# Optimization experiments

Measured on AMD Instinct MI355X. Metric: run time of the kernel, lower is better.

The kernel has to match this reference:

```python
import jax, jax.numpy as jnp
import numpy as np

N_NODES = 100000
N_EDGES = 3200000
N_GRAPHS = 64
IN_DIM = 64
LATENT = 64
DIST_STD = 1.0


def _gcn_conv(x, W, b, src, dst, dinv):
    """PyG GCNConv: out = D^-1/2 (A+I) D^-1/2 (x W) + b, with dinv = deg^-1/2."""
    n = x.shape[0]
    h = x @ W  # [N, out]
    coef = dinv[src] * dinv[dst]  # per-edge norm
    agg = jax.ops.segment_sum(h[src] * coef[:, None], dst, num_segments=n)
    # self-loop contribution with norm dinv[i]^2
    return agg + h * (dinv * dinv)[:, None] + b


def _mean_pool(x, batch, num_graphs):
    sums = jax.ops.segment_sum(x, batch, num_segments=num_graphs)
    cnts = jax.ops.segment_sum(jnp.ones((x.shape[0],), x.dtype), batch, num_segments=num_graphs)
    return sums / jnp.maximum(cnts, 1.0)[:, None]


def setup_inputs() -> dict:
    key = jax.random.key(0)
    ks = jax.random.split(key, 12)
    x = jax.random.normal(ks[0], (N_NODES, IN_DIM), jnp.float32)
    edge_index = jax.random.randint(ks[1], (2, N_EDGES), 0, N_NODES, jnp.int64 if jax.config.jax_enable_x64 else jnp.int32).astype(jnp.int32)
    batch = jnp.sort(jax.random.randint(ks[2], (N_NODES,), 0, N_GRAPHS)).astype(jnp.int32)

    def glorot(k, shape):
        fan_in, fan_out = shape
        s = jnp.sqrt(6.0 / (fan_in + fan_out))
        return jax.random.uniform(k, shape, jnp.float32, -s, s)

    return {
        "x": x, "edge_index": edge_index, "batch": batch,
        "W1m": glorot(ks[3], (IN_DIM, 16)), "b1m": jnp.zeros((16,), jnp.float32),
        "W2m": glorot(ks[4], (16, 32)), "b2m": jnp.zeros((32,), jnp.float32),
        "W3m": glorot(ks[5], (32, LATENT)), "b3m": jnp.zeros((LATENT,), jnp.float32),
        "W1l": glorot(ks[6], (IN_DIM, 16)), "b1l": jnp.zeros((16,), jnp.float32),
        "W2l": glorot(ks[7], (16, 32)), "b2l": jnp.zeros((32,), jnp.float32),
        "W3l": glorot(ks[8], (32, LATENT)), "b3l": jnp.zeros((LATENT,), jnp.float32),
        "Wfc": glorot(ks[9], (LATENT, 160000)), "bfc": jnp.zeros((160000,), jnp.float32),
        "eps": jax.random.normal(ks[10], (N_GRAPHS, LATENT), jnp.float32) * DIST_STD,
    }


def reference(x, edge_index, batch, W1m, b1m, W2m, b2m, W3m, b3m,
              W1l, b1l, W2l, b2l, W3l, b3l, Wfc, bfc, eps):
    src, dst = edge_index[0], edge_index[1]
    n = x.shape[0]
    # degrees include self-loop (+1)
    deg = jax.ops.segment_sum(jnp.ones((src.shape[0],), x.dtype), dst, num_segments=n) + 1.0
    dinv = jax.lax.rsqrt(deg)

    mu = jax.nn.relu(_gcn_conv(x, W1m, b1m, src, dst, dinv))
    mu = jax.nn.relu(_gcn_conv(mu, W2m, b2m, src, dst, dinv))
    mu = jax.nn.relu(_gcn_conv(mu, W3m, b3m, src, dst, dinv))
    mu = _mean_pool(mu, batch, N_GRAPHS)

    log = jax.nn.relu(_gcn_conv(x, W1l, b1l, src, dst, dinv))
    log = jax.nn.relu(_gcn_conv(log, W2l, b2l, src, dst, dinv))
    log = jax.nn.relu(_gcn_conv(log, W3l, b3l, src, dst, dinv))
    logvar = _mean_pool(log, batch, N_GRAPHS)

    # latent sample (training mode): z = mu + eps * exp(0.5*logvar)
    z = mu + eps * jnp.exp(0.5 * logvar)

    # decode: sigmoid(z Wfc + bfc) -> [G, 400, 400]
    output = jax.nn.sigmoid(z @ Wfc + bfc).reshape(-1, 400, 400)
    return output, mu, logvar
```

## Files before the change

### kernel.cpp

```cpp
#include <hip/hip_runtime.h>
#include <hip/hip_bf16.h>

#define N_NODES 100000
#define N_EDGES 3200000
#define N_GRAPHS 64
#define NB 391
#define KCH 8192
#define NCHUNK ((N_EDGES + KCH - 1) / KCH)
#define MAXBKT 10240

__device__ __forceinline__ void atomAddF(float* p, float v) {
    unsafeAtomicAdd(p, v);
}

__device__ __forceinline__ float lo2f(unsigned u) { return __uint_as_float(u << 16); }
__device__ __forceinline__ float hi2f(unsigned u) { return __uint_as_float(u & 0xFFFF0000u); }
__device__ __forceinline__ unsigned pack2(float a, float b) {
    unsigned ha = __bfloat16_as_ushort(__float2bfloat16(a));
    unsigned hb = __bfloat16_as_ushort(__float2bfloat16(b));
    return ha | (hb << 16);
}

__global__ __launch_bounds__(512) void k_binCount(const int* __restrict__ dst,
                                                  int* __restrict__ gcount) {
    __shared__ int hist[NB];
    for (int t = threadIdx.x; t < NB; t += 512) hist[t] = 0;
    __syncthreads();
    int base = blockIdx.x * KCH;
    int cnt = min(KCH, N_EDGES - base);
    for (int i = threadIdx.x; i < cnt; i += 512)
        atomicAdd(&hist[dst[base + i] >> 8], 1);
    __syncthreads();
    for (int t = threadIdx.x; t < NB; t += 512)
        if (hist[t]) atomicAdd(&gcount[t], hist[t]);
}

__global__ __launch_bounds__(512) void k_scanB(const int* __restrict__ gcount,
                                               int* __restrict__ gbase,
                                               int* __restrict__ gcursor,
                                               int* __restrict__ rowptr) {
    __shared__ int s[512];
    int v = (threadIdx.x < NB) ? gcount[threadIdx.x] : 0;
    s[threadIdx.x] = v;
    __syncthreads();
    for (int off = 1; off < 512; off <<= 1) {
        int t = (threadIdx.x >= off) ? s[threadIdx.x - off] : 0;
        __syncthreads();
        s[threadIdx.x] += t;
        __syncthreads();
    }
    if (threadIdx.x < NB) {
        int e = s[threadIdx.x] - v;
        gbase[threadIdx.x] = e;
        gcursor[threadIdx.x] = e;
    }
    if (threadIdx.x == 0) rowptr[N_NODES] = N_EDGES;
}

__global__ __launch_bounds__(512) void k_binA(const int* __restrict__ src,
                                              const int* __restrict__ dst,
                                              int* __restrict__ gcursor,
                                              int* __restrict__ binned) {
    __shared__ int hist[512];
    __shared__ int sc[512];
    __shared__ int sexc[512];
    __shared__ int rbase[512];
    __shared__ int stage[KCH];
    hist[threadIdx.x] = 0;
    __syncthreads();
    int base = blockIdx.x * KCH;
    int cnt = min(KCH, N_EDGES - base);
    int myb[16], mypos[16];
    int nmine = 0;
    for (int i = 0; i < 16; ++i) {
        int idx = i * 512 + threadIdx.x;
        if (idx < cnt) {
            int b = dst[base + idx] >> 8;
            myb[nmine] = b;
            mypos[nmine] = atomicAdd(&hist[b], 1);
            ++nmine;
        }
    }
    __syncthreads();
    int v = hist[threadIdx.x];
    sc[threadIdx.x] = v;
    __syncthreads();
    for (int off = 1; off < 512; off <<= 1) {
        int t = (threadIdx.x >= off) ? sc[threadIdx.x - off] : 0;
        __syncthreads();
        sc[threadIdx.x] += t;
        __syncthreads();
    }
    sexc[threadIdx.x] = sc[threadIdx.x] - v;
    __syncthreads();
    if (threadIdx.x < NB && v > 0)
        rbase[threadIdx.x] = atomicAdd(&gcursor[threadIdx.x], v);
    for (int k = 0; k < nmine; ++k) {
        int e = base + k * 512 + threadIdx.x;
        int p = ((dst[e] & 255) << 24) | src[e];
        stage[sexc[myb[k]] + mypos[k]] = p;
    }
    __syncthreads();
    for (int j = threadIdx.x; j < cnt; j += 512) {
        int lo = 0, hi = NB - 1;
        while (lo < hi) {
            int mid = (lo + hi + 1) >> 1;
            if (sexc[mid] <= j) lo = mid; else hi = mid - 1;
        }
        binned[rbase[lo] + (j - sexc[lo])] = stage[j];
    }
}

__global__ __launch_bounds__(512) void k_passB(const int* __restrict__ gbase,
                                               int* __restrict__ csr,
                                               int* __restrict__ rowptr,
                                               float* __restrict__ dinv) {
    int b = blockIdx.x;
    int rb = gbase[b];
    int re = (b == NB - 1) ? N_EDGES : gbase[b + 1];
    int cnt = re - rb;
    int nbase = b << 8;
    int nn = min(nbase + 256, N_NODES) - nbase;
    __shared__ int stage[MAXBKT];
    __shared__ int nhist[256];
    __shared__ int sc[256];
    __shared__ int ncur[256];
    for (int t = threadIdx.x; t < 256; t += 512) nhist[t] = 0;
    __syncthreads();
    for (int j = threadIdx.x; j < cnt; j += 512) {
        int p = csr[rb + j];
        stage[j] = p;
        atomicAdd(&nhist[((unsigned)p) >> 24], 1);
    }
    __syncthreads();
    if (threadIdx.x < 256) sc[threadIdx.x] = nhist[threadIdx.x];
    __syncthreads();
    for (int off = 1; off < 256; off <<= 1) {
        int t = (threadIdx.x < 256 && threadIdx.x >= off) ? sc[threadIdx.x - off] : 0;
        __syncthreads();
        if (threadIdx.x < 256) sc[threadIdx.x] += t;
        __syncthreads();
    }
    if (threadIdx.x < 256) {
        int e = sc[threadIdx.x] - nhist[threadIdx.x];
        ncur[threadIdx.x] = e;
        if (threadIdx.x < nn) {
            rowptr[nbase + threadIdx.x] = rb + e;
            dinv[nbase + threadIdx.x] = rsqrtf((float)nhist[threadIdx.x] + 1.0f);
        }
    }
    __syncthreads();
    for (int j = threadIdx.x; j < cnt; j += 512) {
        int p = stage[j];
        int slot = atomicAdd(&ncur[((unsigned)p) >> 24], 1);
        csr[rb + slot] = p;
    }
}

template<int LOGW, bool BIAS_RELU, bool OB, bool PRE>
__global__ void __launch_bounds__(256) k_gatherB(
        const int* __restrict__ rowptr, const int* __restrict__ csr,
        const unsigned* __restrict__ in ,
        const float* __restrict__ dinv,
        const float* __restrict__ ba, const float* __restrict__ bb,
        void* __restrict__ out) {
    constexpr int W8 = (1 << LOGW) / 8;
    constexpr int NPB = 256 / W8;
    int n = blockIdx.x * NPB + (threadIdx.x / W8);
    if (n >= N_NODES) return;
    int sub = threadIdx.x % W8;
    const uint4* in4 = (const uint4*)in;
    uint4 u = in4[(size_t)n * W8 + sub];
    float a0 = lo2f(u.x), a1 = hi2f(u.x), a2 = lo2f(u.y), a3 = hi2f(u.y);
    float a4 = lo2f(u.z), a5 = hi2f(u.z), a6 = lo2f(u.w), a7 = hi2f(u.w);
    int j = rowptr[n], end = rowptr[n + 1];
    for (; j + 8 <= end; j += 8) {
        int s0 = csr[j] & 0xFFFFFF;
        int s1 = csr[j + 1] & 0xFFFFFF;
        int s2 = csr[j + 2] & 0xFFFFFF;
        int s3 = csr[j + 3] & 0xFFFFFF;
        int s4 = csr[j + 4] & 0xFFFFFF;
        int s5 = csr[j + 5] & 0xFFFFFF;
        int s6 = csr[j + 6] & 0xFFFFFF;
        int s7 = csr[j + 7] & 0xFFFFFF;
        uint4 v0 = in4[(size_t)s0 * W8 + sub];
        uint4 v1 = in4[(size_t)s1 * W8 + sub];
        uint4 v2 = in4[(size_t)s2 * W8 + sub];
        uint4 v3 = in4[(size_t)s3 * W8 + sub];
        uint4 v4 = in4[(size_t)s4 * W8 + sub];
        uint4 v5 = in4[(size_t)s5 * W8 + sub];
        uint4 v6 = in4[(size_t)s6 * W8 + sub];
        uint4 v7 = in4[(size_t)s7 * W8 + sub];
        a0 += ((lo2f(v0.x) + lo2f(v1.x)) + (lo2f(v2.x) + lo2f(v3.x)))
            + ((lo2f(v4.x) + lo2f(v5.x)) + (lo2f(v6.x) + lo2f(v7.x)));
        a1 += ((hi2f(v0.x) + hi2f(v1.x)) + (hi2f(v2.x) + hi2f(v3.x)))
            + ((hi2f(v4.x) + hi2f(v5.x)) + (hi2f(v6.x) + hi2f(v7.x)));
        a2 += ((lo2f(v0.y) + lo2f(v1.y)) + (lo2f(v2.y) + lo2f(v3.y)))
            + ((lo2f(v4.y) + lo2f(v5.y)) + (lo2f(v6.y) + lo2f(v7.y)));
        a3 += ((hi2f(v0.y) + hi2f(v1.y)) + (hi2f(v2.y) + hi2f(v3.y)))
            + ((hi2f(v4.y) + hi2f(v5.y)) + (hi2f(v6.y) + hi2f(v7.y)));
        a4 += ((lo2f(v0.z) + lo2f(v1.z)) + (lo2f(v2.z) + lo2f(v3.z)))
            + ((lo2f(v4.z) + lo2f(v5.z)) + (lo2f(v6.z) + lo2f(v7.z)));
        a5 += ((hi2f(v0.z) + hi2f(v1.z)) + (hi2f(v2.z) + hi2f(v3.z)))
            + ((hi2f(v4.z) + hi2f(v5.z)) + (hi2f(v6.z) + hi2f(v7.z)));
        a6 += ((lo2f(v0.w) + lo2f(v1.w)) + (lo2f(v2.w) + lo2f(v3.w)))
            + ((lo2f(v4.w) + lo2f(v5.w)) + (lo2f(v6.w) + lo2f(v7.w)));
        a7 += ((hi2f(v0.w) + hi2f(v1.w)) + (hi2f(v2.w) + hi2f(v3.w)))
            + ((hi2f(v4.w) + hi2f(v5.w)) + (hi2f(v6.w) + hi2f(v7.w)));
    }
    for (; j < end; ++j) {
        int s = csr[j] & 0xFFFFFF;
        uint4 v = in4[(size_t)s * W8 + sub];
        a0 += lo2f(v.x); a1 += hi2f(v.x);
        a2 += lo2f(v.y); a3 += hi2f(v.y);
        a4 += lo2f(v.z); a5 += hi2f(v.z);
        a6 += lo2f(v.w); a7 += hi2f(v.w);
    }
    float di = dinv[n];
    a0 *= di; a1 *= di; a2 *= di; a3 *= di;
    a4 *= di; a5 *= di; a6 *= di; a7 *= di;
    if (BIAS_RELU) {
        constexpr int H = (1 << LOGW) / 2;
        int d = sub * 8;
        const float* bp = (d < H) ? (ba + d) : (bb + d - H);
        a0 = fmaxf(a0 + bp[0], 0.0f);
        a1 = fmaxf(a1 + bp[1], 0.0f);
        a2 = fmaxf(a2 + bp[2], 0.0f);
        a3 = fmaxf(a3 + bp[3], 0.0f);
        a4 = fmaxf(a4 + bp[4], 0.0f);
        a5 = fmaxf(a5 + bp[5], 0.0f);
        a6 = fmaxf(a6 + bp[6], 0.0f);
        a7 = fmaxf(a7 + bp[7], 0.0f);
    }
    if (PRE) {
        a0 *= di; a1 *= di; a2 *= di; a3 *= di;
        a4 *= di; a5 *= di; a6 *= di; a7 *= di;
    }
    if (OB) {
        ((uint4*)out)[(size_t)n * W8 + sub] =
            make_uint4(pack2(a0, a1), pack2(a2, a3), pack2(a4, a5), pack2(a6, a7));
    } else {
        constexpr int OUT4 = (1 << LOGW) / 4;
        float4* o4 = (float4*)out;
        o4[(size_t)n * OUT4 + sub * 2]     = make_float4(a0, a1, a2, a3);
        o4[(size_t)n * OUT4 + sub * 2 + 1] = make_float4(a4, a5, a6, a7);
    }
}

template<int IN_W, int OUT_HALF, int A_OFF, int A_W, int B_OFF, bool BR, bool OB, bool DS>
__global__ void k_dense4(const float* __restrict__ in,
                         const float* __restrict__ Wa, const float* __restrict__ ba,
                         const float* __restrict__ Wb, const float* __restrict__ bb,
                         const float* __restrict__ dinv,
                         void* __restrict__ out) {
    __shared__ float sWa[A_W * OUT_HALF];
    __shared__ float sWb[A_W * OUT_HALF];
    __shared__ float sba[OUT_HALF];
    __shared__ float sbb[OUT_HALF];
    for (int t = threadIdx.x; t < A_W * OUT_HALF; t += 256) {
        sWa[t] = Wa[t];
        sWb[t] = Wb[t];
    }
    if (BR && threadIdx.x < OUT_HALF) {
        sba[threadIdx.x] = ba[threadIdx.x];
        sbb[threadIdx.x] = bb[threadIdx.x];
    }
    __syncthreads();
    constexpr int TPN = OUT_HALF / 2;
    int idx = blockIdx.x * 256 + threadIdx.x;
    int n = idx / TPN;
    int q = idx % TPN;
    bool isB = (q * 4) >= OUT_HALF;
    int dd = q * 4 - (isB ? OUT_HALF : 0);
    const float* sW = isB ? sWb : sWa;
    int ko = isB ? B_OFF : A_OFF;
    float4 acc;
    if (BR) {
        const float* bp = isB ? (sbb + dd) : (sba + dd);
        acc = make_float4(bp[0], bp[1], bp[2], bp[3]);
    } else {
        acc = make_float4(0.f, 0.f, 0.f, 0.f);
    }
    const float* row = in + (size_t)n * IN_W + ko;
    #pragma unroll
    for (int k = 0; k < A_W; ++k) {
        float r = row[k];
        float4 wv = *(const float4*)&sW[k * OUT_HALF + dd];
        acc.x = fmaf(r, wv.x, acc.x);
        acc.y = fmaf(r, wv.y, acc.y);
        acc.z = fmaf(r, wv.z, acc.z);
        acc.w = fmaf(r, wv.w, acc.w);
    }
    if (BR) {
        acc.x = fmaxf(acc.x, 0.f); acc.y = fmaxf(acc.y, 0.f);
        acc.z = fmaxf(acc.z, 0.f); acc.w = fmaxf(acc.w, 0.f);
    }
    if (DS) {
        float dn = dinv[n];
        acc.x *= dn; acc.y *= dn; acc.z *= dn; acc.w *= dn;
    }
    if (OB) {
        ((uint2*)out)[idx] = make_uint2(pack2(acc.x, acc.y), pack2(acc.z, acc.w));
    } else {
        ((float4*)out)[idx] = acc;
    }
}

__global__ void k_pool2(const float* __restrict__ h3, const int* __restrict__ batch,
                        float* __restrict__ pool, int* __restrict__ cnt) {
    int g = blockIdx.x >> 2;
    int q = blockIdx.x & 3;
    __shared__ int sb[2];
    if (threadIdx.x < 2) {
        int target = g + threadIdx.x;
        int lo = 0, hi = N_NODES;
        while (lo < hi) {
            int mid = (lo + hi) >> 1;
            if (batch[mid] < target) lo = mid + 1; else hi = mid;
        }
        sb[threadIdx.x] = lo;
    }
    __syncthreads();
    int start = sb[0], end = sb[1];
    int d = threadIdx.x & 127;
    int half = threadIdx.x >> 7;
    float acc = 0.0f;
    for (int n = start + q * 2 + half; n < end; n += 8)
        acc += h3[(size_t)n * 128 + d];
    __shared__ float sred[256];
    sred[threadIdx.x] = acc;
    __syncthreads();
    if (half == 0)
        atomAddF(&pool[g * 128 + d], sred[threadIdx.x] + sred[threadIdx.x + 128]);
    if (threadIdx.x == 0 && q == 0) cnt[g] = end - start;
}

__global__ void k_final(const float* __restrict__ pool, const int* __restrict__ cnt,
                        const float* __restrict__ eps, float* __restrict__ zbuf,
                        float* __restrict__ out_mu, float* __restrict__ out_lv) {
    int idx = blockIdx.x * 256 + threadIdx.x;
    int g = idx >> 6;
    int k = idx & 63;
    float c = fmaxf((float)cnt[g], 1.0f);
    float mu = pool[g * 128 + k] / c;
    float lv = pool[g * 128 + 64 + k] / c;
    zbuf[k * 64 + g] = mu + eps[idx] * __expf(0.5f * lv);
    out_mu[idx] = mu;
    out_lv[idx] = lv;
}

__global__ void __launch_bounds__(256) k_decode(const float* __restrict__ zT,
                                                const float* __restrict__ Wfc,
                                                const float* __restrict__ bfc,
                                                float* __restrict__ out) {
    int j = (blockIdx.x >> 1) * 256 + threadIdx.x;
    int gh = (blockIdx.x & 1) * 32;
    const float* zp = zT + gh;
    float bias = bfc[j];
    float acc[32];
    #pragma unroll
    for (int g = 0; g < 32; ++g) acc[g] = bias;
    #pragma unroll 8
    for (int k = 0; k < 64; ++k) {
        float w = Wfc[(size_t)k * 160000 + j];
        #pragma unroll
        for (int g = 0; g < 32; ++g)
            acc[g] = fmaf(zp[k * 64 + g], w, acc[g]);
    }
    #pragma unroll
    for (int g = 0; g < 32; ++g) {
        float s = 1.0f / (1.0f + __expf(-acc[g]));
        out[(size_t)(gh + g) * 160000 + j] = s;
    }
}

extern "C" void kernel_launch(void* const* d_in, const int* in_sizes, int n_in,
                              void* d_out, int out_size, void* d_ws, size_t ws_size,
                              hipStream_t stream) {
    const float* x     = (const float*)d_in[0];
    const int*   ei    = (const int*)d_in[1];
    const int*   batch = (const int*)d_in[2];
    const float *W1m = (const float*)d_in[3],  *b1m = (const float*)d_in[4];
    const float *W2m = (const float*)d_in[5],  *b2m = (const float*)d_in[6];
    const float *W3m = (const float*)d_in[7],  *b3m = (const float*)d_in[8];
    const float *W1l = (const float*)d_in[9],  *b1l = (const float*)d_in[10];
    const float *W2l = (const float*)d_in[11], *b2l = (const float*)d_in[12];
    const float *W3l = (const float*)d_in[13], *b3l = (const float*)d_in[14];
    const float *Wfc = (const float*)d_in[15], *bfc = (const float*)d_in[16];
    const float *eps = (const float*)d_in[17];

    const int* srcv = ei;
    const int* dstv = ei + N_EDGES;

    char* w = (char*)d_ws;
    auto alloc = [&](size_t bytes) -> char* {
        char* p = w;
        w += (bytes + 255) & ~(size_t)255;
        return p;
    };
    int*   gcount = (int*)  alloc((size_t)NB * 4);
    int*   gbase  = (int*)  alloc((size_t)NB * 4);
    int*   gcursor= (int*)  alloc((size_t)NB * 4);
    int*   rowptr = (int*)  alloc((size_t)(N_NODES + 1) * 4);
    float* dinv   = (float*)alloc((size_t)N_NODES * 4);
    float* pool   = (float*)alloc((size_t)N_GRAPHS * 128 * 4);
    int*   cnt    = (int*)  alloc((size_t)N_GRAPHS * 4);
    float* zbuf   = (float*)alloc((size_t)N_GRAPHS * 64 * 4);
    float* arena = (float*)alloc((size_t)N_NODES * 192 * 4);
    float* A   = arena;
    float* B   = arena + (size_t)N_NODES * 64;
    int*   csr = (int*)(arena + (size_t)N_NODES * 128);
    float* h3  = B;

    float* out    = (float*)d_out;
    float* out_mu = out + 10240000;
    float* out_lv = out + 10240000 + 4096;

    hipMemsetAsync(gcount, 0, (size_t)NB * 4, stream);
    hipMemsetAsync(pool, 0, (size_t)N_GRAPHS * 128 * 4, stream);

    k_binCount<<<NCHUNK, 512, 0, stream>>>(dstv, gcount);
    k_scanB<<<1, 512, 0, stream>>>(gcount, gbase, gcursor, rowptr);
    k_binA<<<NCHUNK, 512, 0, stream>>>(srcv, dstv, gcursor, csr);
    k_passB<<<NB, 512, 0, stream>>>(gbase, csr, rowptr, dinv);

    k_dense4<64, 16, 0, 64, 0, false, true, true><<<N_NODES * 8 / 256, 256, 0, stream>>>(
        x, W1m, b1m, W1l, b1l, dinv, A);
    k_gatherB<5, true, true, true><<<(N_NODES + 63) / 64, 256, 0, stream>>>(
        rowptr, csr, (const unsigned*)A, dinv, b1m, b1l, B);

    k_gatherB<5, false, false, false><<<(N_NODES + 63) / 64, 256, 0, stream>>>(
        rowptr, csr, (const unsigned*)B, dinv, b1m, b1l, A);
    k_dense4<32, 32, 0, 16, 16, true, true, true><<<N_NODES * 16 / 256, 256, 0, stream>>>(
        A, W2m, b2m, W2l, b2l, dinv, B);

    k_gatherB<6, false, false, false><<<(N_NODES + 31) / 32, 256, 0, stream>>>(
        rowptr, csr, (const unsigned*)B, dinv, b1m, b1l, A);
    k_dense4<64, 64, 0, 32, 32, true, false, false><<<N_NODES * 32 / 256, 256, 0, stream>>>(
        A, W3m, b3m, W3l, b3l, dinv, h3);

    k_pool2<<<N_GRAPHS * 4, 256, 0, stream>>>(h3, batch, pool, cnt);
    k_final<<<16, 256, 0, stream>>>(pool, cnt, eps, zbuf, out_mu, out_lv);

    k_decode<<<1250, 256, 0, stream>>>(zbuf, Wfc, bfc, out);
}
```

Measured before the change: 496.2 us.

## Fuse layer-3 gather, dense transform and mean-pool into one kernel

Replaces the third-layer gather, the dense layer-3 matmul and the pooling kernel with a single kernel. Each block aggregates neighbours for 32 nodes, applies the combined W3 transform in shared memory, and accumulates pooled sums with run-length atomics keyed by the sorted batch ids. This avoids writing and re-reading the 64-wide aggregate and the 128-wide h3 arrays in global memory and removes two launches. Graph node counts are now computed by binary search inside k_final instead of in the pooling kernel. The cost is more atomics on the pool buffer and heavier per-block shared memory.

```diff
diff --git a/kernel.cpp b/kernel.cpp
--- a/kernel.cpp
+++ b/kernel.cpp
@@ -247,6 +247,148 @@
     }
 }
 
+__global__ void __launch_bounds__(256) k_gd3(
+        const int* __restrict__ rowptr, const int* __restrict__ csr,
+        const unsigned* __restrict__ in,
+        const float* __restrict__ dinv,
+        const float* __restrict__ W3m, const float* __restrict__ b3m,
+        const float* __restrict__ W3l, const float* __restrict__ b3l,
+        const int* __restrict__ batch,
+        float* __restrict__ pool) {
+    __shared__ float s_ali[32 * 132];
+    __shared__ float agg[32 * 68];
+    __shared__ float sbias[128];
+    __shared__ int   sbatch[32];
+    float* sWall = s_ali;
+    float* h3s   = s_ali;
+
+    for (int t = threadIdx.x; t < 4096; t += 256) {
+        int k = t >> 7, D = t & 127;
+        sWall[t] = (D < 64) ? W3m[k * 64 + D] : W3l[k * 64 + (D - 64)];
+    }
+    if (threadIdx.x < 128)
+        sbias[threadIdx.x] = (threadIdx.x < 64) ? b3m[threadIdx.x]
+                                                : b3l[threadIdx.x - 64];
+    int nbase = blockIdx.x * 32;
+    if (threadIdx.x < 32) sbatch[threadIdx.x] = batch[nbase + threadIdx.x];
+
+    int ln  = threadIdx.x >> 3;
+    int sub = threadIdx.x & 7;
+    int n = nbase + ln;
+    const uint4* in4 = (const uint4*)in;
+    uint4 u = in4[(size_t)n * 8 + sub];
+    float a0 = lo2f(u.x), a1 = hi2f(u.x), a2 = lo2f(u.y), a3 = hi2f(u.y);
+    float a4 = lo2f(u.z), a5 = hi2f(u.z), a6 = lo2f(u.w), a7 = hi2f(u.w);
+    int j = rowptr[n], end = rowptr[n + 1];
+    for (; j + 8 <= end; j += 8) {
+        int s0 = csr[j] & 0xFFFFFF;
+        int s1 = csr[j + 1] & 0xFFFFFF;
+        int s2 = csr[j + 2] & 0xFFFFFF;
+        int s3 = csr[j + 3] & 0xFFFFFF;
+        int s4 = csr[j + 4] & 0xFFFFFF;
+        int s5 = csr[j + 5] & 0xFFFFFF;
+        int s6 = csr[j + 6] & 0xFFFFFF;
+        int s7 = csr[j + 7] & 0xFFFFFF;
+        uint4 v0 = in4[(size_t)s0 * 8 + sub];
+        uint4 v1 = in4[(size_t)s1 * 8 + sub];
+        uint4 v2 = in4[(size_t)s2 * 8 + sub];
+        uint4 v3 = in4[(size_t)s3 * 8 + sub];
+        uint4 v4 = in4[(size_t)s4 * 8 + sub];
+        uint4 v5 = in4[(size_t)s5 * 8 + sub];
+        uint4 v6 = in4[(size_t)s6 * 8 + sub];
+        uint4 v7 = in4[(size_t)s7 * 8 + sub];
+        a0 += ((lo2f(v0.x) + lo2f(v1.x)) + (lo2f(v2.x) + lo2f(v3.x)))
+            + ((lo2f(v4.x) + lo2f(v5.x)) + (lo2f(v6.x) + lo2f(v7.x)));
+        a1 += ((hi2f(v0.x) + hi2f(v1.x)) + (hi2f(v2.x) + hi2f(v3.x)))
+            + ((hi2f(v4.x) + hi2f(v5.x)) + (hi2f(v6.x) + hi2f(v7.x)));
+        a2 += ((lo2f(v0.y) + lo2f(v1.y)) + (lo2f(v2.y) + lo2f(v3.y)))
+            + ((lo2f(v4.y) + lo2f(v5.y)) + (lo2f(v6.y) + lo2f(v7.y)));
+        a3 += ((hi2f(v0.y) + hi2f(v1.y)) + (hi2f(v2.y) + hi2f(v3.y)))
+            + ((hi2f(v4.y) + hi2f(v5.y)) + (hi2f(v6.y) + hi2f(v7.y)));
+        a4 += ((lo2f(v0.z) + lo2f(v1.z)) + (lo2f(v2.z) + lo2f(v3.z)))
+            + ((lo2f(v4.z) + lo2f(v5.z)) + (lo2f(v6.z) + lo2f(v7.z)));
+        a5 += ((hi2f(v0.z) + hi2f(v1.z)) + (hi2f(v2.z) + hi2f(v3.z)))
+            + ((hi2f(v4.z) + hi2f(v5.z)) + (hi2f(v6.z) + hi2f(v7.z)));
+        a6 += ((lo2f(v0.w) + lo2f(v1.w)) + (lo2f(v2.w) + lo2f(v3.w)))
+            + ((lo2f(v4.w) + lo2f(v5.w)) + (lo2f(v6.w) + lo2f(v7.w)));
+        a7 += ((hi2f(v0.w) + hi2f(v1.w)) + (hi2f(v2.w) + hi2f(v3.w)))
+            + ((hi2f(v4.w) + hi2f(v5.w)) + (hi2f(v6.w) + hi2f(v7.w)));
+    }
+    for (; j < end; ++j) {
+        int s = csr[j] & 0xFFFFFF;
+        uint4 v = in4[(size_t)s * 8 + sub];
+        a0 += lo2f(v.x); a1 += hi2f(v.x);
+        a2 += lo2f(v.y); a3 += hi2f(v.y);
+        a4 += lo2f(v.z); a5 += hi2f(v.z);
+        a6 += lo2f(v.w); a7 += hi2f(v.w);
+    }
+    float di = dinv[n];
+    a0 *= di; a1 *= di; a2 *= di; a3 *= di;
+    a4 *= di; a5 *= di; a6 *= di; a7 *= di;
+    {
+        float* ap = &agg[ln * 68 + sub * 8];
+        *(float4*)&ap[0] = make_float4(a0, a1, a2, a3);
+        *(float4*)&ap[4] = make_float4(a4, a5, a6, a7);
+    }
+    __syncthreads();
+
+    int ln2 = threadIdx.x >> 3;
+    int q   = threadIdx.x & 7;
+    int Dbase = q * 16;
+    int koff = (q >= 4) ? 32 : 0;
+    float4 acc4[4];
+    #pragma unroll
+    for (int i4 = 0; i4 < 4; ++i4)
+        acc4[i4] = *(const float4*)&sbias[Dbase + i4 * 4];
+    const float* ag = &agg[ln2 * 68 + koff];
+    #pragma unroll
+    for (int k = 0; k < 32; ++k) {
+        float r = ag[k];
+        const float* wr = &sWall[k * 128 + Dbase];
+        #pragma unroll
+        for (int t4 = 0; t4 < 4; ++t4) {
+            int ii = (t4 + q) & 3;
+            float4 wv = *(const float4*)&wr[ii * 4];
+            acc4[ii].x = fmaf(r, wv.x, acc4[ii].x);
+            acc4[ii].y = fmaf(r, wv.y, acc4[ii].y);
+            acc4[ii].z = fmaf(r, wv.z, acc4[ii].z);
+            acc4[ii].w = fmaf(r, wv.w, acc4[ii].w);
+        }
+    }
+    #pragma unroll
+    for (int i4 = 0; i4 < 4; ++i4) {
+        acc4[i4].x = fmaxf(acc4[i4].x, 0.f);
+        acc4[i4].y = fmaxf(acc4[i4].y, 0.f);
+        acc4[i4].z = fmaxf(acc4[i4].z, 0.f);
+        acc4[i4].w = fmaxf(acc4[i4].w, 0.f);
+    }
+    __syncthreads();
+
+    {
+        float* hp = &h3s[ln2 * 132 + Dbase];
+        #pragma unroll
+        for (int i4 = 0; i4 < 4; ++i4)
+            *(float4*)&hp[i4 * 4] = acc4[i4];
+    }
+    __syncthreads();
+    {
+        int d  = threadIdx.x & 127;
+        int r0 = (threadIdx.x >> 7) * 16;
+        float run = 0.f;
+        int gcur = sbatch[r0];
+        for (int nn = r0; nn < r0 + 16; ++nn) {
+            int g = sbatch[nn];
+            if (g != gcur) {
+                atomAddF(&pool[gcur * 128 + d], run);
+                run = 0.f;
+                gcur = g;
+            }
+            run += h3s[nn * 132 + d];
+        }
+        atomAddF(&pool[gcur * 128 + d], run);
+    }
+}
+
 template<int IN_W, int OUT_HALF, int A_OFF, int A_W, int B_OFF, bool BR, bool OB, bool DS>
 __global__ void k_dense4(const float* __restrict__ in,
                          const float* __restrict__ Wa, const float* __restrict__ ba,
@@ -306,42 +448,30 @@
     }
 }
 
-__global__ void k_pool2(const float* __restrict__ h3, const int* __restrict__ batch,
-                        float* __restrict__ pool, int* __restrict__ cnt) {
-    int g = blockIdx.x >> 2;
-    int q = blockIdx.x & 3;
-    __shared__ int sb[2];
-    if (threadIdx.x < 2) {
-        int target = g + threadIdx.x;
+__global__ void k_final(const float* __restrict__ pool, const int* __restrict__ batch,
+                        const float* __restrict__ eps, float* __restrict__ zbuf,
+                        float* __restrict__ out_mu, float* __restrict__ out_lv) {
+    __shared__ int sb[5];
+    int g0 = blockIdx.x * 4;
+    if (threadIdx.x < 5) {
+        int target = g0 + threadIdx.x;
         int lo = 0, hi = N_NODES;
-        while (lo < hi) {
-            int mid = (lo + hi) >> 1;
-            if (batch[mid] < target) lo = mid + 1; else hi = mid;
+        if (target >= N_GRAPHS) {
+            lo = N_NODES;
+        } else {
+            while (lo < hi) {
+                int mid = (lo + hi) >> 1;
+                if (batch[mid] < target) lo = mid + 1; else hi = mid;
+            }
         }
         sb[threadIdx.x] = lo;
     }
     __syncthreads();
-    int start = sb[0], end = sb[1];
-    int d = threadIdx.x & 127;
-    int half = threadIdx.x >> 7;
-    float acc = 0.0f;
-    for (int n = start + q * 2 + half; n < end; n += 8)
-        acc += h3[(size_t)n * 128 + d];
-    __shared__ float sred[256];
-    sred[threadIdx.x] = acc;
-    __syncthreads();
-    if (half == 0)
-        atomAddF(&pool[g * 128 + d], sred[threadIdx.x] + sred[threadIdx.x + 128]);
-    if (threadIdx.x == 0 && q == 0) cnt[g] = end - start;
-}
-
-__global__ void k_final(const float* __restrict__ pool, const int* __restrict__ cnt,
-                        const float* __restrict__ eps, float* __restrict__ zbuf,
-                        float* __restrict__ out_mu, float* __restrict__ out_lv) {
     int idx = blockIdx.x * 256 + threadIdx.x;
     int g = idx >> 6;
     int k = idx & 63;
-    float c = fmaxf((float)cnt[g], 1.0f);
+    int gl = threadIdx.x >> 6;
+    float c = fmaxf((float)(sb[gl + 1] - sb[gl]), 1.0f);
     float mu = pool[g * 128 + k] / c;
     float lv = pool[g * 128 + 64 + k] / c;
     zbuf[k * 64 + g] = mu + eps[idx] * __expf(0.5f * lv);
@@ -404,13 +534,11 @@
     int*   rowptr = (int*)  alloc((size_t)(N_NODES + 1) * 4);
     float* dinv   = (float*)alloc((size_t)N_NODES * 4);
     float* pool   = (float*)alloc((size_t)N_GRAPHS * 128 * 4);
-    int*   cnt    = (int*)  alloc((size_t)N_GRAPHS * 4);
     float* zbuf   = (float*)alloc((size_t)N_GRAPHS * 64 * 4);
     float* arena = (float*)alloc((size_t)N_NODES * 192 * 4);
     float* A   = arena;
     float* B   = arena + (size_t)N_NODES * 64;
     int*   csr = (int*)(arena + (size_t)N_NODES * 128);
-    float* h3  = B;
 
     float* out    = (float*)d_out;
     float* out_mu = out + 10240000;
@@ -434,13 +562,10 @@
     k_dense4<32, 32, 0, 16, 16, true, true, true><<<N_NODES * 16 / 256, 256, 0, stream>>>(
         A, W2m, b2m, W2l, b2l, dinv, B);
 
-    k_gatherB<6, false, false, false><<<(N_NODES + 31) / 32, 256, 0, stream>>>(
-        rowptr, csr, (const unsigned*)B, dinv, b1m, b1l, A);
-    k_dense4<64, 64, 0, 32, 32, true, false, false><<<N_NODES * 32 / 256, 256, 0, stream>>>(
-        A, W3m, b3m, W3l, b3l, dinv, h3);
-
-    k_pool2<<<N_GRAPHS * 4, 256, 0, stream>>>(h3, batch, pool, cnt);
-    k_final<<<16, 256, 0, stream>>>(pool, cnt, eps, zbuf, out_mu, out_lv);
+    k_gd3<<<N_NODES / 32, 256, 0, stream>>>(
+        rowptr, csr, (const unsigned*)B, dinv, W3m, b3m, W3l, b3l, batch, pool);
+
+    k_final<<<16, 256, 0, stream>>>(pool, batch, eps, zbuf, out_mu, out_lv);
 
     k_decode<<<1250, 256, 0, stream>>>(zbuf, Wfc, bfc, out);
 }
```

Measured after the change: 1.299 ms. 2.62x slower.
